# Performance work log

Hardware: AMD Instinct MI355X
Metric: run time of the kernel (lower is better)

Reference implementation:

```python
import jax, jax.numpy as jnp
import numpy as np

B, T, D, H, NL, V = 2, 2048, 512, 8, 4, 32000
HD = D // H
EPS = 1e-5


def _ln(x, g, b):
    mu = jnp.mean(x, axis=-1, keepdims=True)
    var = jnp.var(x, axis=-1, keepdims=True)
    return (x - mu) * jax.lax.rsqrt(var + EPS) * g + b


def setup_inputs() -> dict:
    key = jax.random.key(0)
    ks = jax.random.split(key, 16)
    f = lambda k, shp: jax.random.normal(k, shp, jnp.float32) * 0.02
    return {
        "token_ids": jax.random.randint(ks[0], (B, T), 0, V),
        "labels": jax.random.randint(ks[1], (B, T), 0, V),
        "tok_emb": f(ks[2], (V, D)),
        "pos_emb": f(ks[3], (T, D)),
        "Wq": f(ks[4], (NL, H, D, HD)),
        "Wk": f(ks[5], (NL, H, D, HD)),
        "Wv": f(ks[6], (NL, H, D, HD)),
        "Wo": f(ks[7], (NL, D, D)),
        "bo": jnp.zeros((NL, D), jnp.float32),
        "ln1_g": jnp.ones((NL, D), jnp.float32),
        "ln1_b": jnp.zeros((NL, D), jnp.float32),
        "ln2_g": jnp.ones((NL, D), jnp.float32),
        "ln2_b": jnp.zeros((NL, D), jnp.float32),
        "W1": f(ks[8], (NL, D, 4 * D)),
        "b1": jnp.zeros((NL, 4 * D), jnp.float32),
        "W2": f(ks[9], (NL, 4 * D, D)),
        "b2": jnp.zeros((NL, D), jnp.float32),
        "lnf_g": jnp.ones((D,), jnp.float32),
        "lnf_b": jnp.zeros((D,), jnp.float32),
        "Wp": f(ks[10], (D, V)),
        "bp": jnp.zeros((V,), jnp.float32),
    }


def reference(token_ids, labels, tok_emb, pos_emb, Wq, Wk, Wv, Wo, bo,
              ln1_g, ln1_b, ln2_g, ln2_b, W1, b1, W2, b2, lnf_g, lnf_b, Wp, bp):
    x = tok_emb[token_ids] + pos_emb[:T]            # (B, T, D)
    causal = jnp.tril(jnp.ones((T, T), bool))       # tril buffer
    scale = D ** -0.5                               # NOTE: source scales by dim_embed, not head_size
    for l in range(NL):
        xn = _ln(x, ln1_g[l], ln1_b[l])
        q = jnp.einsum('btd,hde->bhte', xn, Wq[l])  # (B, H, T, HD)
        k = jnp.einsum('btd,hde->bhte', xn, Wk[l])
        v = jnp.einsum('btd,hde->bhte', xn, Wv[l])
        w = jnp.einsum('bhte,bhse->bhts', q, k) * scale
        w = jnp.where(causal, w, -jnp.inf)
        w = jax.nn.softmax(w, axis=-1)
        o = jnp.einsum('bhts,bhse->bhte', w, v)     # (B, H, T, HD)
        o = o.transpose(0, 2, 1, 3).reshape(B, T, D)  # concat heads
        x = x + o @ Wo[l] + bo[l]
        xn = _ln(x, ln2_g[l], ln2_b[l])
        x = x + jax.nn.relu(xn @ W1[l] + b1[l]) @ W2[l] + b2[l]
    x = _ln(x, lnf_g, lnf_b)
    logits = x @ Wp + bp                            # (B, T, V)
    logits2d = logits.reshape(B * T, V)
    logp = jax.nn.log_softmax(logits2d, axis=-1)
    loss = -jnp.mean(logp[jnp.arange(B * T), labels.reshape(B * T)])
    return logits2d, loss
```

## Files before the change

### kernel.cpp

```cpp
#include <hip/hip_runtime.h>
#include <hip/hip_bf16.h>
#include <math.h>

#define B_ 2
#define T_ 2048
#define D_ 512
#define H_ 8
#define NL_ 4
#define V_ 32000
#define HD_ 64
#define BT_ (B_*T_)
#define EPS_ 1e-5f
#define SCALE_ 0.04419417382415922f
#define NEGBIG -1e30f

typedef __bf16 bf16x8 __attribute__((ext_vector_type(8)));
typedef float  f32x4  __attribute__((ext_vector_type(4)));

__device__ __forceinline__ unsigned short f2bf(float f) {
  union { float f; unsigned u; } v; v.f = f;
  unsigned r = v.u + 0x7fff + ((v.u >> 16) & 1);
  return (unsigned short)(r >> 16);
}

__device__ __forceinline__ void gl_lds16(const void* g, void* l) {
  __builtin_amdgcn_global_load_lds(
      (const __attribute__((address_space(1))) void*)g,
      (__attribute__((address_space(3))) void*)l, 16, 0, 0);
}

#define WAITVM(n) asm volatile("s_waitcnt vmcnt(" #n ")" ::: "memory")
#define WAITLG0   asm volatile("s_waitcnt lgkmcnt(0)" ::: "memory")

__global__ __launch_bounds__(256) void embed_kernel(
    const int* __restrict__ ids, const float* __restrict__ tok,
    const float* __restrict__ pos, float* __restrict__ x)
{
  int i = blockIdx.x * 256 + threadIdx.x;
  int d4 = i & (D_/4 - 1);
  int bt = i >> 7;
  int t  = bt & (T_ - 1);
  const float4 a = reinterpret_cast<const float4*>(tok + (size_t)ids[bt] * D_)[d4];
  const float4 p = reinterpret_cast<const float4*>(pos + (size_t)t * D_)[d4];
  float4 r; r.x = a.x + p.x; r.y = a.y + p.y; r.z = a.z + p.z; r.w = a.w + p.w;
  reinterpret_cast<float4*>(x)[i] = r;
}

__global__ __launch_bounds__(256) void ln_kernel(
    const float* __restrict__ x, const float* __restrict__ g,
    const float* __restrict__ b, unsigned short* __restrict__ out)
{
  int row  = blockIdx.x * 4 + (threadIdx.x >> 6);
  int lane = threadIdx.x & 63;
  const float4* xr = reinterpret_cast<const float4*>(x + (size_t)row * D_);
  float4 v0 = xr[lane], v1 = xr[lane + 64];
  float s = v0.x + v0.y + v0.z + v0.w + v1.x + v1.y + v1.z + v1.w;
  float q = v0.x*v0.x + v0.y*v0.y + v0.z*v0.z + v0.w*v0.w
          + v1.x*v1.x + v1.y*v1.y + v1.z*v1.z + v1.w*v1.w;
  #pragma unroll
  for (int off = 1; off < 64; off <<= 1) {
    s += __shfl_xor(s, off);
    q += __shfl_xor(q, off);
  }
  float mean = s * (1.0f / D_);
  float var  = q * (1.0f / D_) - mean * mean;
  float rs   = rsqrtf(var + EPS_);
  const float4* g4 = reinterpret_cast<const float4*>(g);
  const float4* b4 = reinterpret_cast<const float4*>(b);
  float4 gv0 = g4[lane], gv1 = g4[lane + 64];
  float4 bv0 = b4[lane], bv1 = b4[lane + 64];
  ushort4 p0, p1;
  p0.x = f2bf((v0.x - mean) * rs * gv0.x + bv0.x);
  p0.y = f2bf((v0.y - mean) * rs * gv0.y + bv0.y);
  p0.z = f2bf((v0.z - mean) * rs * gv0.z + bv0.z);
  p0.w = f2bf((v0.w - mean) * rs * gv0.w + bv0.w);
  p1.x = f2bf((v1.x - mean) * rs * gv1.x + bv1.x);
  p1.y = f2bf((v1.y - mean) * rs * gv1.y + bv1.y);
  p1.z = f2bf((v1.z - mean) * rs * gv1.z + bv1.z);
  p1.w = f2bf((v1.w - mean) * rs * gv1.w + bv1.w);
  unsigned short* orow = out + (size_t)row * D_;
  *reinterpret_cast<ushort4*>(orow + lane * 4)       = p0;
  *reinterpret_cast<ushort4*>(orow + 256 + lane * 4) = p1;
}

__global__ __launch_bounds__(256) void transpose_cast(
    const float* __restrict__ src, unsigned short* __restrict__ dst,
    int C, int R, long sstride, long dstride)
{
  src += (size_t)blockIdx.z * sstride;
  dst += (size_t)blockIdx.z * dstride;
  __shared__ float t[32][33];
  int r0 = blockIdx.x * 32, c0 = blockIdx.y * 32;
  int tx = threadIdx.x & 31, ty = threadIdx.x >> 5;
  #pragma unroll
  for (int i = 0; i < 4; i++)
    t[ty + i*8][tx] = src[(size_t)(r0 + ty + i*8) * C + c0 + tx];
  __syncthreads();
  #pragma unroll
  for (int i = 0; i < 4; i++)
    dst[(size_t)(c0 + ty + i*8) * R + r0 + tx] = f2bf(t[tx][ty + i*8]);
}

__global__ __launch_bounds__(256) void qkvw_transpose(
    const float* __restrict__ Wq, const float* __restrict__ Wk,
    const float* __restrict__ Wv, unsigned short* __restrict__ dst)
{
  int z = blockIdx.z; int l = z / 24; int rem = z % 24; int mat = rem >> 3; int h = rem & 7;
  const float* W = (mat == 0 ? Wq : (mat == 1 ? Wk : Wv)) + ((size_t)(l * 8 + h)) * D_ * HD_;
  unsigned short* d = dst + ((size_t)l * 1536 + mat * 512 + h * 64) * D_;
  __shared__ float t[32][33];
  int d0 = blockIdx.x * 32, e0 = blockIdx.y * 32;
  int tx = threadIdx.x & 31, ty = threadIdx.x >> 5;
  #pragma unroll
  for (int i = 0; i < 4; i++)
    t[ty + i*8][tx] = W[(size_t)(d0 + ty + i*8) * HD_ + e0 + tx];
  __syncthreads();
  #pragma unroll
  for (int i = 0; i < 4; i++)
    d[(size_t)(e0 + ty + i*8) * D_ + d0 + tx] = f2bf(t[tx][ty + i*8]);
}

__global__ __launch_bounds__(512, 4) void gemm_logits(
    const unsigned short* __restrict__ A,
    const unsigned short* __restrict__ Bt,
    int K, const float* __restrict__ bias,
    float* __restrict__ outF, int ldc,
    float2* __restrict__ ms, int npan)
{
  __shared__ __align__(16) char smem[73728];
  unsigned short* Abase = (unsigned short*)smem;
  unsigned short* Bbase = (unsigned short*)(smem + 24576);
  float* E = (float*)smem;

  const int tid = threadIdx.x;
  const int lane = tid & 63;
  const int lr = lane & 15, g = lane >> 4;
  const int wv = tid >> 6, wm = wv >> 2, wn = wv & 3;

  const int gx = gridDim.x;
  int id = blockIdx.y * gx + blockIdx.x;
  const int nwg = gx * gridDim.y;
  if ((nwg & 7) == 0) { const int q = nwg >> 3; id = (id & 7) * q + (id >> 3); }
  const int bm = (id % gx) * 128, bn = (id / gx) * 256, bnp = id / gx;

  const int schk = (lane & 3) ^ ((lane >> 3) & 3);
  const unsigned short* Ab = A  + (size_t)(bm + wv*16 + (lane >> 2)) * K + schk * 8;
  const unsigned short* Bb = Bt + (size_t)(bn + wv*16 + (lane >> 2)) * K + schk * 8;

#define STAGEL(s, sl)                                                       \
  { const int kof_ = (s) * 32;                                              \
    gl_lds16(Ab + kof_,                 Abase + (sl)*4096 + wv*512);        \
    gl_lds16(Bb + kof_,                 Bbase + (sl)*8192 + wv*512);        \
    gl_lds16(Bb + (size_t)128*K + kof_, Bbase + (sl)*8192 + 4096 + wv*512); }

  f32x4 acc[4][4];
  #pragma unroll
  for (int m = 0; m < 4; m++)
    #pragma unroll
    for (int n = 0; n < 4; n++)
      acc[m][n] = (f32x4){0.f, 0.f, 0.f, 0.f};

  const int nt = K >> 5;
  STAGEL(0, 0); STAGEL(1, 1);

  const int slotx = (g ^ ((lr >> 1) & 3)) << 3;

  for (int t = 0; t < nt; ++t) {
    const int s = t + 2;
    const int st = t % 3;
    __builtin_amdgcn_sched_barrier(0);
    if      (s < nt)  { const int ss = s % 3; STAGEL(s, ss); WAITVM(6); }
    else if (s == nt) { WAITVM(3); }
    else              { WAITVM(0); }
    __builtin_amdgcn_sched_barrier(0);
    __builtin_amdgcn_s_barrier();
    __builtin_amdgcn_sched_barrier(0);

    const unsigned short* Ac = Abase + st*4096;
    const unsigned short* Bc = Bbase + st*8192;
    bf16x8 af[4], bfr[4];
    #pragma unroll
    for (int m = 0; m < 4; m++)
      af[m] = *reinterpret_cast<const bf16x8*>(&Ac[(wm*64 + m*16 + lr) * 32 + slotx]);
    #pragma unroll
    for (int n = 0; n < 4; n++)
      bfr[n] = *reinterpret_cast<const bf16x8*>(&Bc[(wn*64 + n*16 + lr) * 32 + slotx]);
    __builtin_amdgcn_s_setprio(1);
    #pragma unroll
    for (int m = 0; m < 4; m++)
      #pragma unroll
      for (int n = 0; n < 4; n++)
        acc[m][n] = __builtin_amdgcn_mfma_f32_16x16x32_bf16(af[m], bfr[n], acc[m][n], 0, 0, 0);
    __builtin_amdgcn_s_setprio(0);
    __builtin_amdgcn_sched_barrier(0);
    __builtin_amdgcn_s_barrier();
  }
#undef STAGEL

  #pragma unroll
  for (int n = 0; n < 4; n++) {
    const float bv = bias ? bias[bn + wn*64 + n*16 + lr] : 0.f;
    #pragma unroll
    for (int m = 0; m < 4; m++)
      #pragma unroll
      for (int r = 0; r < 4; r++)
        acc[m][n][r] += bv;
  }

  if (ms) {
    #pragma unroll
    for (int m = 0; m < 4; m++) {
      float vmax[4] = {NEGBIG, NEGBIG, NEGBIG, NEGBIG};
      #pragma unroll
      for (int n = 0; n < 4; n++)
        #pragma unroll
        for (int r = 0; r < 4; r++)
          vmax[r] = fmaxf(vmax[r], acc[m][n][r]);
      #pragma unroll
      for (int r = 0; r < 4; r++) {
        #pragma unroll
        for (int off = 1; off < 16; off <<= 1)
          vmax[r] = fmaxf(vmax[r], __shfl_xor(vmax[r], off));
      }
      float vsum[4] = {0.f, 0.f, 0.f, 0.f};
      #pragma unroll
      for (int n = 0; n < 4; n++)
        #pragma unroll
        for (int r = 0; r < 4; r++)
          vsum[r] += __expf(acc[m][n][r] - vmax[r]);
      #pragma unroll
      for (int r = 0; r < 4; r++) {
        #pragma unroll
        for (int off = 1; off < 16; off <<= 1)
          vsum[r] += __shfl_xor(vsum[r], off);
      }
      if (lr == 0) {
        #pragma unroll
        for (int r = 0; r < 4; r++)
          ms[(size_t)(bm + wm*64 + m*16 + g*4 + r) * npan + bnp*4 + wn] =
              make_float2(vmax[r], vsum[r]);
      }
    }
  }

  #pragma unroll
  for (int c = 0; c < 2; ++c) {
    __syncthreads();
    if (wm == c) {
      #pragma unroll
      for (int m = 0; m < 4; m++)
        #pragma unroll
        for (int n = 0; n < 4; n++)
          #pragma unroll
          for (int r = 0; r < 4; r++)
            E[(m*16 + g*4 + r) * 260 + wn*64 + n*16 + lr] = acc[m][n][r];
    }
    __syncthreads();
    #pragma unroll
    for (int rep = 0; rep < 8; rep++) {
      const int row = rep*8 + wv;
      f32x4 v = *reinterpret_cast<const f32x4*>(&E[row*260 + lane*4]);
      __builtin_nontemporal_store(
          v, reinterpret_cast<f32x4*>(&outF[(size_t)(bm + c*64 + row) * ldc + bn + lane*4]));
    }
  }
}

template<int BM_T, int BN_T, int WM, int WN>
__global__ __launch_bounds__(256) void gemm_pipe(
    const unsigned short* __restrict__ A,
    const unsigned short* __restrict__ Bt,
    int K,
    const float* __restrict__ bias,
    const float* __restrict__ resid,
    float* __restrict__ outF,
    unsigned short* __restrict__ outH,
    int ldc, int relu)
{
  constexpr int BKp = 32;
  constexpr int ALOADS = BM_T / 64;
  constexpr int BLOADS = BN_T / 64;
  constexpr int LOADS  = ALOADS + BLOADS;
  constexpr int MR = BM_T / (16 * WM);
  constexpr int NR = BN_T / (16 * WN);
  __shared__ __align__(16) unsigned short As[3][BM_T * BKp];
  __shared__ __align__(16) unsigned short Bs[3][BN_T * BKp];

  const int tid = threadIdx.x;
  const int lane = tid & 63, wv = tid >> 6;
  const int lr = lane & 15, g = lane >> 4;

  const int gx = gridDim.x;
  int id = blockIdx.y * gx + blockIdx.x;
  const int nwg = gx * gridDim.y;
  if ((nwg & 7) == 0) {
    const int q = nwg >> 3;
    id = (id & 7) * q + (id >> 3);
  }
  const int bm = (id % gx) * BM_T, bn = (id / gx) * BN_T;

  const int m0w = (wv / WN) * (BM_T / WM);
  const int n0w = (wv % WN) * (BN_T / WN);

  const int schk = (lane & 3) ^ ((lane >> 3) & 3);
  const unsigned short* Ab = A  + (size_t)(bm + wv*(BM_T/4) + (lane >> 2)) * K + schk * 8;
  const unsigned short* Bb = Bt + (size_t)(bn + wv*(BN_T/4) + (lane >> 2)) * K + schk * 8;

#define STAGEP(s, sl)                                                           \
  { const int kof_ = (s) * BKp;                                                 \
    unsigned short* Ad_ = As[sl] + wv*(ALOADS*512);                             \
    unsigned short* Bd_ = Bs[sl] + wv*(BLOADS*512);                             \
    _Pragma("unroll")                                                           \
    for (int i_ = 0; i_ < ALOADS; ++i_)                                         \
      gl_lds16(Ab + (size_t)(i_*16)*K + kof_, Ad_ + i_*512);                    \
    _Pragma("unroll")                                                           \
    for (int i_ = 0; i_ < BLOADS; ++i_)                                         \
      gl_lds16(Bb + (size_t)(i_*16)*K + kof_, Bd_ + i_*512); }

  f32x4 acc[MR][NR];
  #pragma unroll
  for (int m = 0; m < MR; m++)
    #pragma unroll
    for (int n = 0; n < NR; n++)
      acc[m][n] = (f32x4){0.f, 0.f, 0.f, 0.f};

  const int nt = K >> 5;
  STAGEP(0, 0); STAGEP(1, 1);

  const int slotx = (g ^ ((lr >> 1) & 3)) << 3;

  for (int t = 0; t < nt; ++t) {
    const int s = t + 2;
    const int st = t % 3;
    __builtin_amdgcn_sched_barrier(0);
    if (s < nt) {
      const int ss = s % 3;
      STAGEP(s, ss);
      if constexpr (LOADS == 4) WAITVM(8); else if constexpr (LOADS == 3) WAITVM(6); else WAITVM(4);
    } else if (s == nt) {
      if constexpr (LOADS == 4) WAITVM(4); else if constexpr (LOADS == 3) WAITVM(3); else WAITVM(2);
    } else {
      WAITVM(0);
    }
    __builtin_amdgcn_sched_barrier(0);
    __builtin_amdgcn_s_barrier();
    __builtin_amdgcn_sched_barrier(0);

    const unsigned short* Ac = As[st];
    const unsigned short* Bc = Bs[st];
    bf16x8 af[MR], bfr[NR];
    #pragma unroll
    for (int m = 0; m < MR; m++)
      af[m] = *reinterpret_cast<const bf16x8*>(&Ac[(m0w + m*16 + lr) * BKp + slotx]);
    #pragma unroll
    for (int n = 0; n < NR; n++)
      bfr[n] = *reinterpret_cast<const bf16x8*>(&Bc[(n0w + n*16 + lr) * BKp + slotx]);
    __builtin_amdgcn_s_setprio(1);
    #pragma unroll
    for (int m = 0; m < MR; m++)
      #pragma unroll
      for (int n = 0; n < NR; n++)
        acc[m][n] = __builtin_amdgcn_mfma_f32_16x16x32_bf16(af[m], bfr[n], acc[m][n], 0, 0, 0);
    __builtin_amdgcn_s_setprio(0);

    __builtin_amdgcn_sched_barrier(0);
    __builtin_amdgcn_s_barrier();
  }
#undef STAGEP

  const int cr = g * 4;
  const int cc = lr;
  #pragma unroll
  for (int m = 0; m < MR; m++) {
    #pragma unroll
    for (int n = 0; n < NR; n++) {
      int row = bm + m0w + m*16 + cr;
      int col = bn + n0w + n*16 + cc;
      f32x4 a = acc[m][n];
      #pragma unroll
      for (int r = 0; r < 4; r++) {
        float v = a[r];
        if (bias)  v += bias[col];
        if (resid) v += resid[(size_t)(row + r) * ldc + col];
        if (relu)  v = fmaxf(v, 0.f);
        if (outF)  outF[(size_t)(row + r) * ldc + col] = v;
        if (outH)  outH[(size_t)(row + r) * ldc + col] = f2bf(v);
      }
    }
  }
}

__global__ __launch_bounds__(512) void attn_mfma(
    const unsigned short* __restrict__ qkv,
    unsigned short* __restrict__ o)
{
  __shared__ __align__(16) unsigned short Ks[2][64*64];
  __shared__ __align__(16) unsigned short Vt[2][64*64];
  __shared__ __align__(16) unsigned short Ps[8][16*64];

  const int qb = (int)gridDim.x - 1 - (int)blockIdx.x;
  const int bh = blockIdx.y, bb = bh >> 3, hh = bh & 7;
  const int tid = threadIdx.x, lane = tid & 63, wv = tid >> 6;
  const int lr = lane & 15, g = lane >> 4;

  const unsigned short* qp = qkv + ((size_t)(bb*T_ + qb*128))*1536 + hh*64;
  const unsigned short* kp = qkv + ((size_t)bb*T_)*1536 + 512  + hh*64;
  const unsigned short* vp = qkv + ((size_t)bb*T_)*1536 + 1024 + hh*64;

  bf16x8 qf[2];
  qf[0] = *reinterpret_cast<const bf16x8*>(qp + (size_t)(wv*16 + lr)*1536 + g*8);
  qf[1] = *reinterpret_cast<const bf16x8*>(qp + (size_t)(wv*16 + lr)*1536 + 32 + g*8);

  const int krow = wv*8 + (lane >> 3);
  const int khb  = (lane & 7) ^ (lane >> 3);

#define STAGE_K(s0_, buf_)                                           \
  gl_lds16(kp + (size_t)((s0_)*64 + krow)*1536 + khb*8,              \
           (void*)(Ks[buf_] + wv*512));

  uint4 uvr;
#define LOAD_V(s0_)                                                  \
  uvr = *reinterpret_cast<const uint4*>(                             \
      vp + (size_t)((s0_)*64 + lane)*1536 + wv*8);

  f32x4 ov[4];
  #pragma unroll
  for (int n = 0; n < 4; n++) ov[n] = (f32x4){0.f, 0.f, 0.f, 0.f};
  float mrow[4] = {NEGBIG, NEGBIG, NEGBIG, NEGBIG};
  float lrow[4] = {0.f, 0.f, 0.f, 0.f};

  const int smax = 2*qb + 1;
  STAGE_K(0, 0);
  LOAD_V(0);

  for (int s0 = 0; s0 <= smax; ++s0) {
    const int cur = s0 & 1;
    WAITVM(0);
    __builtin_amdgcn_sched_barrier(0);
    {
      union { uint4 v; unsigned short e[8]; } uv; uv.v = uvr;
      #pragma unroll
      for (int j = 0; j < 8; j++)
        Vt[cur][(wv*8 + j)*64 + (((lane >> 3) ^ j) << 3) + (lane & 7)] = uv.e[j];
    }
    WAITLG0;
    __builtin_amdgcn_sched_barrier(0);
    __builtin_amdgcn_s_barrier();
    __builtin_amdgcn_sched_barrier(0);

    if (s0 < smax) {
      STAGE_K(s0 + 1, cur ^ 1);
      LOAD_V(s0 + 1);
    }

    f32x4 sf[4];
    #pragma unroll
    for (int n = 0; n < 4; n++) sf[n] = (f32x4){0.f, 0.f, 0.f, 0.f};
    __builtin_amdgcn_s_setprio(1);
    #pragma unroll
    for (int kk = 0; kk < 2; kk++) {
      #pragma unroll
      for (int n = 0; n < 4; n++) {
        const bf16x8 kf = *reinterpret_cast<const bf16x8*>(
            &Ks[cur][(n*16 + lr)*64 + (((kk*4 + g) ^ (lr & 7)) << 3)]);
        sf[n] = __builtin_amdgcn_mfma_f32_16x16x32_bf16(qf[kk], kf, sf[n], 0, 0, 0);
      }
    }
    __builtin_amdgcn_s_setprio(0);

    float sv[4][4];
    #pragma unroll
    for (int n = 0; n < 4; n++)
      #pragma unroll
      for (int r = 0; r < 4; r++) {
        const int kvg = s0*64 + n*16 + lr;
        const int qg  = qb*128 + wv*16 + g*4 + r;
        sv[n][r] = (kvg > qg) ? NEGBIG : sf[n][r] * SCALE_;
      }

    float aa[4];
    #pragma unroll
    for (int r = 0; r < 4; r++) {
      float pm = fmaxf(fmaxf(sv[0][r], sv[1][r]), fmaxf(sv[2][r], sv[3][r]));
      pm = fmaxf(pm, __shfl_xor(pm, 1));
      pm = fmaxf(pm, __shfl_xor(pm, 2));
      pm = fmaxf(pm, __shfl_xor(pm, 4));
      pm = fmaxf(pm, __shfl_xor(pm, 8));
      float mn = fmaxf(mrow[r], pm);
      aa[r] = __expf(mrow[r] - mn);
      mrow[r] = mn;
    }
    float rs[4] = {0.f, 0.f, 0.f, 0.f};
    #pragma unroll
    for (int n = 0; n < 4; n++)
      #pragma unroll
      for (int r = 0; r < 4; r++) {
        float p = __expf(sv[n][r] - mrow[r]);
        rs[r] += p;
        Ps[wv][(g*4 + r)*64 + ((((n << 1) + (lr >> 3)) ^ ((g*4 + r) & 7)) << 3) + (lr & 7)] = f2bf(p);
      }
    #pragma unroll
    for (int r = 0; r < 4; r++) {
      float s = rs[r];
      s += __shfl_xor(s, 1); s += __shfl_xor(s, 2);
      s += __shfl_xor(s, 4); s += __shfl_xor(s, 8);
      lrow[r] = lrow[r]*aa[r] + s;
    }
    #pragma unroll
    for (int n = 0; n < 4; n++)
      #pragma unroll
      for (int r = 0; r < 4; r++)
        ov[n][r] *= aa[r];

    __builtin_amdgcn_s_setprio(1);
    #pragma unroll
    for (int kk = 0; kk < 2; kk++) {
      const bf16x8 pf = *reinterpret_cast<const bf16x8*>(
          &Ps[wv][lr*64 + (((kk*4 + g) ^ (lr & 7)) << 3)]);
      #pragma unroll
      for (int n = 0; n < 4; n++) {
        const bf16x8 vf = *reinterpret_cast<const bf16x8*>(
            &Vt[cur][(n*16 + lr)*64 + (((kk*4 + g) ^ (lr & 7)) << 3)]);
        ov[n] = __builtin_amdgcn_mfma_f32_16x16x32_bf16(pf, vf, ov[n], 0, 0, 0);
      }
    }
    __builtin_amdgcn_s_setprio(0);
    __builtin_amdgcn_sched_barrier(0);
    __builtin_amdgcn_s_barrier();
  }
#undef STAGE_K
#undef LOAD_V

  #pragma unroll
  for (int r = 0; r < 4; r++) {
    float inv = 1.0f / lrow[r];
    size_t row = (size_t)(bb*T_ + qb*128 + wv*16 + g*4 + r);
    #pragma unroll
    for (int n = 0; n < 4; n++)
      o[row*D_ + hh*64 + n*16 + lr] = f2bf(ov[n][r] * inv);
  }
}

__global__ __launch_bounds__(256) void loss_merge_kernel(
    const float2* __restrict__ ms, const float* __restrict__ logits,
    const int* __restrict__ labels, float* __restrict__ rowloss, int npan)
{
  const int tid = threadIdx.x, lane = tid & 63, wid = tid >> 6;
  const int row = blockIdx.x * 4 + wid;
  float M = NEGBIG, S = 0.f;
  const float2* p = ms + (size_t)row * npan;
  for (int i = lane; i < npan; i += 64) {
    float2 e = p[i];
    float Mn = fmaxf(M, e.x);
    S = S * __expf(M - Mn) + e.y * __expf(e.x - Mn);
    M = Mn;
  }
  #pragma unroll
  for (int off = 1; off < 64; off <<= 1) {
    float Mo = __shfl_xor(M, off), So = __shfl_xor(S, off);
    float Mn = fmaxf(M, Mo);
    S = S * __expf(M - Mn) + So * __expf(Mo - Mn);
    M = Mn;
  }
  if (lane == 0)
    rowloss[row] = logits[(size_t)row * V_ + labels[row]] - M - logf(S);
}

__global__ __launch_bounds__(256) void loss_final_kernel(
    const float* __restrict__ rowloss, float* __restrict__ out)
{
  __shared__ float red[4];
  const int tid = threadIdx.x, lane = tid & 63, wid = tid >> 6;
  float s = 0.f;
  for (int i = tid; i < BT_; i += 256) s += rowloss[i];
  #pragma unroll
  for (int off = 1; off < 64; off <<= 1) s += __shfl_xor(s, off);
  if (lane == 0) red[wid] = s;
  __syncthreads();
  if (tid == 0) out[0] = -(red[0] + red[1] + red[2] + red[3]) * (1.0f / BT_);
}

extern "C" void kernel_launch(void* const* d_in, const int* in_sizes, int n_in,
                              void* d_out, int out_size, void* d_ws, size_t ws_size,
                              hipStream_t stream)
{
  (void)in_sizes; (void)n_in; (void)out_size; (void)ws_size;
  const int*   ids    = (const int*)d_in[0];
  const int*   labels = (const int*)d_in[1];
  const float* tok    = (const float*)d_in[2];
  const float* pos    = (const float*)d_in[3];
  const float* Wq     = (const float*)d_in[4];
  const float* Wk     = (const float*)d_in[5];
  const float* Wv     = (const float*)d_in[6];
  const float* Wo     = (const float*)d_in[7];
  const float* bo     = (const float*)d_in[8];
  const float* ln1g   = (const float*)d_in[9];
  const float* ln1b   = (const float*)d_in[10];
  const float* ln2g   = (const float*)d_in[11];
  const float* ln2b   = (const float*)d_in[12];
  const float* W1     = (const float*)d_in[13];
  const float* b1     = (const float*)d_in[14];
  const float* W2     = (const float*)d_in[15];
  const float* b2     = (const float*)d_in[16];
  const float* lnfg   = (const float*)d_in[17];
  const float* lnfb   = (const float*)d_in[18];
  const float* Wp     = (const float*)d_in[19];
  const float* bp     = (const float*)d_in[20];

  float* out = (float*)d_out;
  char* base = (char*)d_ws;
  float*          x       = (float*)(base + 0);
  unsigned short* xn      = (unsigned short*)(base + 8388608);
  float*          rowloss = (float*)(base + 12582912);
  unsigned short* WqkvT   = (unsigned short*)(base + 12599296);
  unsigned short* W1T     = (unsigned short*)(base + 18890752);
  unsigned short* W2T     = (unsigned short*)(base + 27279360);
  unsigned short* WoT     = (unsigned short*)(base + 35667968);
  unsigned short* qkvh    = (unsigned short*)(base + 37765120);
  unsigned short* ob      = (unsigned short*)(base + 50348032);
  unsigned short* h1      = (unsigned short*)(base + 54542336);
  unsigned short* WpT     = (unsigned short*)(base + 37765120);
  float2*         msbuf   = (float2*)(base + 12599296);

  embed_kernel<<<BT_ * D_ / 4 / 256, 256, 0, stream>>>(ids, tok, pos, x);

  qkvw_transpose<<<dim3(16, 2, 96), 256, 0, stream>>>(Wq, Wk, Wv, WqkvT);
  transpose_cast<<<dim3(16, 64, 4), 256, 0, stream>>>(W1, W1T, 2048, 512, 1048576, 1048576);
  transpose_cast<<<dim3(64, 16, 4), 256, 0, stream>>>(W2, W2T, 512, 2048, 1048576, 1048576);
  transpose_cast<<<dim3(16, 16, 4), 256, 0, stream>>>(Wo, WoT, 512, 512, 262144, 262144);

  for (int l = 0; l < NL_; l++) {
    ln_kernel<<<BT_ / 4, 256, 0, stream>>>(x, ln1g + l * D_, ln1b + l * D_, xn);
    gemm_pipe<64,64,2,2><<<dim3(64, 24), 256, 0, stream>>>(
        xn, WqkvT + (size_t)l * 1536 * 512, 512, nullptr, nullptr, nullptr, qkvh, 1536, 0);
    attn_mfma<<<dim3(T_ / 128, B_ * H_), 512, 0, stream>>>(qkvh, ob);
    gemm_pipe<64,64,2,2><<<dim3(64, 8), 256, 0, stream>>>(
        ob, WoT + (size_t)l * 512 * 512, 512, bo + l * D_, x, x, nullptr, D_, 0);
    ln_kernel<<<BT_ / 4, 256, 0, stream>>>(x, ln2g + l * D_, ln2b + l * D_, xn);
    gemm_pipe<64,64,2,2><<<dim3(64, 32), 256, 0, stream>>>(
        xn, W1T + (size_t)l * 2048 * 512, 512, b1 + l * 4 * D_, nullptr, nullptr, h1, 4 * D_, 1);
    gemm_pipe<64,64,2,2><<<dim3(64, 8), 256, 0, stream>>>(
        h1, W2T + (size_t)l * 512 * 2048, 2048, b2 + l * D_, x, x, nullptr, D_, 0);
  }

  transpose_cast<<<dim3(16, 1000, 1), 256, 0, stream>>>(Wp, WpT, 32000, 512, 0, 0);
  ln_kernel<<<BT_ / 4, 256, 0, stream>>>(x, lnfg, lnfb, xn);
  gemm_logits<<<dim3(32, 125), 512, 0, stream>>>(
      xn, WpT, 512, bp, out, V_, msbuf, 500);

  loss_merge_kernel<<<BT_ / 4, 256, 0, stream>>>(msbuf, out, labels, rowloss, 500);
  loss_final_kernel<<<1, 256, 0, stream>>>(rowloss, out + (size_t)BT_ * V_);
}
```

Measured before the change: 991.3 us.

## Split long causal attention query blocks across two workgroups with merge kernel

Query blocks 8-15 of causal attention have their key range split in half. Each half is computed by a separate workgroup that writes unnormalized partial outputs plus row max and sum to scratch. A new merge kernel combines the two halves with log-sum-exp rescaling. A block ordering table schedules the heaviest work first. The aim is to shorten the tail and balance load across 384 workgroups instead of 256, at the cost of an extra launch and fp32 scratch traffic.

```diff
diff --git a/kernel.cpp b/kernel.cpp
--- a/kernel.cpp
+++ b/kernel.cpp
@@ -392,14 +392,22 @@
 
 __global__ __launch_bounds__(512) void attn_mfma(
     const unsigned short* __restrict__ qkv,
-    unsigned short* __restrict__ o)
+    unsigned short* __restrict__ o,
+    float* __restrict__ Opart,
+    float2* __restrict__ ml)
 {
   __shared__ __align__(16) unsigned short Ks[2][64*64];
   __shared__ __align__(16) unsigned short Vt[2][64*64];
   __shared__ __align__(16) unsigned short Ps[8][16*64];
 
-  const int qb = (int)gridDim.x - 1 - (int)blockIdx.x;
+  static const unsigned char ord[24] = {7,22,23,20,21,6,18,19,16,17,5,14,15,12,13,4,10,11,8,9,3,2,1,0};
+  const int slot = ord[blockIdx.x];
   const int bh = blockIdx.y, bb = bh >> 3, hh = bh & 7;
+  int qb, it0, itn, half;
+  if (slot < 8) { qb = slot; it0 = 0; itn = 2*qb + 2; half = -1; }
+  else { const int p = slot - 8; qb = 8 + (p >> 1); half = p & 1;
+         const int nh = qb + 1; it0 = half * nh; itn = nh; }
+
   const int tid = threadIdx.x, lane = tid & 63, wv = tid >> 6;
   const int lr = lane & 15, g = lane >> 4;
 
@@ -429,12 +437,12 @@
   float mrow[4] = {NEGBIG, NEGBIG, NEGBIG, NEGBIG};
   float lrow[4] = {0.f, 0.f, 0.f, 0.f};
 
-  const int smax = 2*qb + 1;
-  STAGE_K(0, 0);
-  LOAD_V(0);
-
-  for (int s0 = 0; s0 <= smax; ++s0) {
-    const int cur = s0 & 1;
+  STAGE_K(it0, 0);
+  LOAD_V(it0);
+
+  for (int ii = 0; ii < itn; ++ii) {
+    const int s0 = it0 + ii;
+    const int cur = ii & 1;
     WAITVM(0);
     __builtin_amdgcn_sched_barrier(0);
     {
@@ -448,7 +456,7 @@
     __builtin_amdgcn_s_barrier();
     __builtin_amdgcn_sched_barrier(0);
 
-    if (s0 < smax) {
+    if (ii + 1 < itn) {
       STAGE_K(s0 + 1, cur ^ 1);
       LOAD_V(s0 + 1);
     }
@@ -531,13 +539,57 @@
 #undef STAGE_K
 #undef LOAD_V
 
-  #pragma unroll
-  for (int r = 0; r < 4; r++) {
-    float inv = 1.0f / lrow[r];
-    size_t row = (size_t)(bb*T_ + qb*128 + wv*16 + g*4 + r);
-    #pragma unroll
-    for (int n = 0; n < 4; n++)
-      o[row*D_ + hh*64 + n*16 + lr] = f2bf(ov[n][r] * inv);
+  if (half < 0) {
+    #pragma unroll
+    for (int r = 0; r < 4; r++) {
+      float inv = 1.0f / lrow[r];
+      size_t row = (size_t)(bb*T_ + qb*128 + wv*16 + g*4 + r);
+      #pragma unroll
+      for (int n = 0; n < 4; n++)
+        o[row*D_ + hh*64 + n*16 + lr] = f2bf(ov[n][r] * inv);
+    }
+  } else {
+    const int blk = bh*8 + (qb - 8);
+    float* Od = Opart + ((size_t)blk*2 + half)*128*64;
+    #pragma unroll
+    for (int r = 0; r < 4; r++) {
+      const int rloc = wv*16 + g*4 + r;
+      #pragma unroll
+      for (int n = 0; n < 4; n++)
+        Od[rloc*64 + n*16 + lr] = ov[n][r];
+      if (lr == 0)
+        ml[((size_t)blk*2 + half)*128 + rloc] = make_float2(mrow[r], lrow[r]);
+    }
+  }
+}
+
+__global__ __launch_bounds__(256) void attn_merge(
+    const float* __restrict__ Opart, const float2* __restrict__ ml,
+    unsigned short* __restrict__ o)
+{
+  const int blk = blockIdx.x;
+  const int bh = blk >> 3, qb = (blk & 7) + 8;
+  const int bb = bh >> 3, hh = bh & 7;
+  const int tid = threadIdx.x;
+  const int row = tid >> 1, ch = (tid & 1) * 32;
+  const float* O0 = Opart + ((size_t)blk*2 + 0)*128*64;
+  const float* O1 = Opart + ((size_t)blk*2 + 1)*128*64;
+  const float2 a = ml[(size_t)blk*2*128 + row];
+  const float2 b = ml[((size_t)blk*2 + 1)*128 + row];
+  const float M  = fmaxf(a.x, b.x);
+  const float e0 = __expf(a.x - M), e1 = __expf(b.x - M);
+  const float inv = 1.0f / (a.y*e0 + b.y*e1);
+  unsigned short* orow = o + ((size_t)(bb*T_ + qb*128 + row))*D_ + hh*64 + ch;
+  #pragma unroll
+  for (int c = 0; c < 32; c += 4) {
+    f32x4 v0 = *reinterpret_cast<const f32x4*>(&O0[row*64 + ch + c]);
+    f32x4 v1 = *reinterpret_cast<const f32x4*>(&O1[row*64 + ch + c]);
+    ushort4 pk;
+    pk.x = f2bf((v0[0]*e0 + v1[0]*e1) * inv);
+    pk.y = f2bf((v0[1]*e0 + v1[1]*e1) * inv);
+    pk.z = f2bf((v0[2]*e0 + v1[2]*e1) * inv);
+    pk.w = f2bf((v0[3]*e0 + v1[3]*e1) * inv);
+    *reinterpret_cast<ushort4*>(&orow[c]) = pk;
   }
 }
 
@@ -619,6 +671,8 @@
   unsigned short* qkvh    = (unsigned short*)(base + 37765120);
   unsigned short* ob      = (unsigned short*)(base + 50348032);
   unsigned short* h1      = (unsigned short*)(base + 54542336);
+  float*          Opart   = (float*)(base + 54542336);
+  float2*         mlbuf   = (float2*)(base + 62930944);
   unsigned short* WpT     = (unsigned short*)(base + 37765120);
   float2*         msbuf   = (float2*)(base + 12599296);
 
@@ -633,7 +687,8 @@
     ln_kernel<<<BT_ / 4, 256, 0, stream>>>(x, ln1g + l * D_, ln1b + l * D_, xn);
     gemm_pipe<64,64,2,2><<<dim3(64, 24), 256, 0, stream>>>(
         xn, WqkvT + (size_t)l * 1536 * 512, 512, nullptr, nullptr, nullptr, qkvh, 1536, 0);
-    attn_mfma<<<dim3(T_ / 128, B_ * H_), 512, 0, stream>>>(qkvh, ob);
+    attn_mfma<<<dim3(24, B_ * H_), 512, 0, stream>>>(qkvh, ob, Opart, mlbuf);
+    attn_merge<<<128, 256, 0, stream>>>(Opart, mlbuf, ob);
     gemm_pipe<64,64,2,2><<<dim3(64, 8), 256, 0, stream>>>(
         ob, WoT + (size_t)l * 512 * 512, 512, bo + l * D_, x, x, nullptr, D_, 0);
     ln_kernel<<<BT_ / 4, 256, 0, stream>>>(x, ln2g + l * D_, ln2b + l * D_, xn);
```

Result: faster. 928.5 us (-6.3%).
